# Kernel optimization log

Hardware: AMD Instinct MI355X
Metric: run time of the kernel (lower is better)

The kernel has to match this reference:

```python
import jax, jax.numpy as jnp
import numpy as np

NUM_HEADS = 8
LN_EPS = 1e-5


def setup_inputs() -> dict:
    key = jax.random.key(0)
    ks = jax.random.split(key, 5)
    B, C, H, W = 4, 256, 48, 48
    scale = 1.0 / np.sqrt(C)
    return {
        "x": jax.random.normal(ks[0], (B, C, H, W), dtype=jnp.float32),
        "Wq": jax.random.normal(ks[1], (C, C), dtype=jnp.float32) * scale,
        "Wk": jax.random.normal(ks[2], (C, C), dtype=jnp.float32) * scale,
        "Wv": jax.random.normal(ks[3], (C, C), dtype=jnp.float32) * scale,
        "Wo": jax.random.normal(ks[4], (C, C), dtype=jnp.float32) * scale,
        "gamma": jnp.ones((C,), dtype=jnp.float32),
        "beta": jnp.zeros((C,), dtype=jnp.float32),
    }


def reference(x, Wq, Wk, Wv, Wo, gamma, beta):
    B, C, H, W = x.shape
    hd = C // NUM_HEADS
    N = H * W
    xf = x.reshape(B, C, N)  # [B, C, N]
    # 1x1 conv (no bias) == channel matmul, then split heads: [B, h, d, N]
    def proj(Wm):
        return jnp.einsum('oc,bcn->bon', Wm, xf).reshape(B, NUM_HEADS, hd, N)
    q = proj(Wq)
    k = proj(Wk)
    v = proj(Wv)
    # scores[b,h,i,j] = sum_d q[b,h,d,i] k[b,h,d,j] / sqrt(hd)
    scores = jnp.einsum('bhdi,bhdj->bhij', q, k) / jnp.sqrt(jnp.float32(hd))
    attn = jax.nn.softmax(scores, axis=-1)  # [B, h, N, N]
    # attended[b,h,d,i] = sum_j v[b,h,d,j] attn[b,h,i,j]
    attended = jnp.einsum('bhdj,bhij->bhdi', v, attn).reshape(B, C, H, W)
    out = jnp.einsum('oc,bchw->bohw', Wo, attended) + x
    # LayerNorm over channels (applied in NHWC layout in original)
    mu = out.mean(axis=1, keepdims=True)
    var = out.var(axis=1, keepdims=True)
    out = (out - mu) * jax.lax.rsqrt(var + LN_EPS)
    out = out * gamma[None, :, None, None] + beta[None, :, None, None]
    return out
```

## Files before the change

### kernel.cpp

```cpp
#include <hip/hip_runtime.h>

#define DEVI __device__ __forceinline__

typedef __bf16 bf16x8 __attribute__((ext_vector_type(8)));
typedef float f32x4 __attribute__((ext_vector_type(4)));

#define QSCALE 0.25503488f

#if __has_builtin(__builtin_amdgcn_exp2f)
#define EXP2(x) __builtin_amdgcn_exp2f(x)
#else
#define EXP2(x) __expf(0.69314718055994531f * (x))
#endif

DEVI unsigned short bfbits(float f) {
  union { __bf16 h; unsigned short u; } x;
  x.h = (__bf16)f;
  return x.u;
}
DEVI unsigned packbf2(float a, float b) {
  return (unsigned)bfbits(a) | ((unsigned)bfbits(b) << 16);
}
DEVI float bflo(unsigned u) { return __uint_as_float(u << 16); }
DEVI float bfhi(unsigned u) { return __uint_as_float(u & 0xffff0000u); }

DEVI void gload16(const unsigned short* g, void* l) {
  __builtin_amdgcn_global_load_lds((__attribute__((address_space(1))) const unsigned*)g,
                                   (__attribute__((address_space(3))) unsigned*)l, 16, 0, 0);
}

__global__ __launch_bounds__(256) void k_prep_x(const float* __restrict__ x,
                                                unsigned short* __restrict__ xT) {
  __shared__ float tile[64][65];
  const int b = blockIdx.x, n0 = blockIdx.y * 64, c0 = blockIdx.z * 64;
  const int t = threadIdx.x, tn = t & 63, tg = t >> 6;
  const float* xp = x + ((size_t)b * 256 + c0) * 2304 + n0;
#pragma unroll
  for (int i = 0; i < 16; ++i) {
    const int c = tg * 16 + i;
    tile[c][tn] = xp[(size_t)c * 2304 + tn];
  }
  __syncthreads();
  unsigned short* op = xT + ((size_t)b * 2304 + n0) * 256 + c0;
#pragma unroll
  for (int i = 0; i < 16; ++i) {
    const int n = tg * 16 + i;
    op[(size_t)n * 256 + tn] = bfbits(tile[tn][n]);
  }
}

__global__ __launch_bounds__(256) void k_prep_w(const float* __restrict__ Wq,
                                                const float* __restrict__ Wk,
                                                const float* __restrict__ Wv,
                                                const float* __restrict__ Wo,
                                                unsigned short* __restrict__ dst) {
  const float* src = blockIdx.y == 0 ? Wq : blockIdx.y == 1 ? Wk : blockIdx.y == 2 ? Wv : Wo;
  unsigned short* d = dst + (size_t)blockIdx.y * 65536;
  const int i = (blockIdx.x * 256 + threadIdx.x) * 4;
  const float4 v = *(const float4*)(src + i);
  uint2 u;
  u.x = packbf2(v.x, v.y);
  u.y = packbf2(v.z, v.w);
  *(uint2*)(d + i) = u;
}

__global__ __launch_bounds__(256) void k_proj_qk(const unsigned short* __restrict__ xT,
                                                 const unsigned short* __restrict__ Wb,
                                                 unsigned short* __restrict__ qT,
                                                 unsigned short* __restrict__ kT) {
  __shared__ __align__(16) unsigned char wlds[16384];
  const unsigned short* W = Wb + (blockIdx.z ? 65536 : 0);
  unsigned short* outp = blockIdx.z ? kT : qT;
  const float scale = blockIdx.z ? 1.0f : QSCALE;
  const int l = threadIdx.x & 63, w = threadIdx.x >> 6;
  const int lr = l & 15, lg = l >> 4;
  const int row0 = blockIdx.x * 128 + w * 32;
  const int col0 = blockIdx.y * 32;
  {
    const int t = threadIdx.x;
    const int row = t >> 3;
    const int cj0 = (t & 7) * 4;
#pragma unroll
    for (int i = 0; i < 4; ++i) {
      const int cj = cj0 + i;
      const uint4 v = *(const uint4*)(W + (size_t)(col0 + row) * 256 + cj * 8);
      *(uint4*)(wlds + row * 512 + ((cj * 16) ^ ((row & 7) << 4))) = v;
    }
  }
  __syncthreads();

  f32x4 acc[2][2];
#pragma unroll
  for (int i = 0; i < 2; ++i)
#pragma unroll
    for (int j = 0; j < 2; ++j) acc[i][j] = (f32x4){0.f, 0.f, 0.f, 0.f};
  for (int ks = 0; ks < 8; ++ks) {
    const int c = ks * 32 + lg * 8;
    bf16x8 a[2], bfr[2];
#pragma unroll
    for (int nt = 0; nt < 2; ++nt)
      a[nt] = *(const bf16x8*)(xT + (size_t)(row0 + nt * 16 + lr) * 256 + c);
#pragma unroll
    for (int ot = 0; ot < 2; ++ot) {
      const int brow = ot * 16 + lr;
      bfr[ot] = *(const bf16x8*)(wlds + brow * 512 + (((ks * 4 + lg) * 16) ^ ((brow & 7) << 4)));
    }
#pragma unroll
    for (int nt = 0; nt < 2; ++nt)
#pragma unroll
      for (int ot = 0; ot < 2; ++ot)
        acc[nt][ot] = __builtin_amdgcn_mfma_f32_16x16x32_bf16(a[nt], bfr[ot], acc[nt][ot], 0, 0, 0);
  }
#pragma unroll
  for (int nt = 0; nt < 2; ++nt)
#pragma unroll
    for (int ot = 0; ot < 2; ++ot)
#pragma unroll
      for (int r = 0; r < 4; ++r) {
        const int n = row0 + nt * 16 + lg * 4 + r;
        const int o = col0 + ot * 16 + lr;
        outp[(size_t)n * 256 + o] = bfbits(acc[nt][ot][r] * scale);
      }
}

__global__ __launch_bounds__(256) void k_proj_v(const unsigned short* __restrict__ xT,
                                                const unsigned short* __restrict__ Wv,
                                                unsigned short* __restrict__ vN) {
  __shared__ __align__(16) unsigned char wlds[32768];
  const int l = threadIdx.x & 63, w = threadIdx.x >> 6;
  const int lr = l & 15, lg = l >> 4;
  const int rowbase = blockIdx.x * 64;
  const int col0 = blockIdx.y * 32;
  {
    const int t = threadIdx.x;
    const int row = t >> 2;
    const int cj0 = (t & 3) * 8;
#pragma unroll
    for (int i = 0; i < 8; ++i) {
      const int cj = cj0 + i;
      const uint4 v = *(const uint4*)(Wv + (size_t)(rowbase + row) * 256 + cj * 8);
      *(uint4*)(wlds + row * 512 + ((cj * 16) ^ ((row & 7) << 4))) = v;
    }
  }
  __syncthreads();

  f32x4 acc[2];
  acc[0] = (f32x4){0.f, 0.f, 0.f, 0.f};
  acc[1] = (f32x4){0.f, 0.f, 0.f, 0.f};
  for (int ks = 0; ks < 8; ++ks) {
    const int c = ks * 32 + lg * 8;
    bf16x8 a, bfr[2];
    const int arow = w * 16 + lr;
    a = *(const bf16x8*)(wlds + arow * 512 + (((ks * 4 + lg) * 16) ^ ((arow & 7) << 4)));
#pragma unroll
    for (int nt = 0; nt < 2; ++nt)
      bfr[nt] = *(const bf16x8*)(xT + (size_t)(col0 + nt * 16 + lr) * 256 + c);
#pragma unroll
    for (int nt = 0; nt < 2; ++nt)
      acc[nt] = __builtin_amdgcn_mfma_f32_16x16x32_bf16(a, bfr[nt], acc[nt], 0, 0, 0);
  }
  const int b = blockIdx.y / 72, nb = (blockIdx.y % 72) * 32;
#pragma unroll
  for (int nt = 0; nt < 2; ++nt)
#pragma unroll
    for (int r = 0; r < 4; ++r) {
      const int o = rowbase + w * 16 + lg * 4 + r;
      const int n = nb + nt * 16 + lr;
      vN[(size_t)b * 589824 + (size_t)o * 2304 + n] = bfbits(acc[nt][r]);
    }
}

template <bool DIRECT>
__global__ __launch_bounds__(256) void k_attn(const unsigned short* __restrict__ qT,
                                              const unsigned short* __restrict__ kT,
                                              const unsigned short* __restrict__ vN,
                                              unsigned short* __restrict__ partO,
                                              float* __restrict__ partS,
                                              unsigned short* __restrict__ attT,
                                              int tpc) {
  __shared__ __align__(16) unsigned char sm[32768];
  const int l = threadIdx.x & 63, w = threadIdx.x >> 6;
  const int lr = l & 15, lg = l >> 4;
  const int bh = blockIdx.y, b = bh >> 3, h = bh & 7;
  const int i0 = blockIdx.x * 128 + w * 32;
  const int c = blockIdx.z, t0 = c * tpc;
  unsigned char* smw = sm + w * 4096;

  bf16x8 qf[2];
#pragma unroll
  for (int it = 0; it < 2; ++it)
    qf[it] = *(const bf16x8*)(qT + (size_t)(b * 2304 + i0 + it * 16 + lr) * 256 + h * 32 + lg * 8);

  bf16x8 ones;
#pragma unroll
  for (int e = 0; e < 8; ++e) ones[e] = (__bf16)1.0f;

  f32x4 oacc[2][2];
#pragma unroll
  for (int i = 0; i < 2; ++i)
#pragma unroll
    for (int j = 0; j < 2; ++j) oacc[i][j] = (f32x4){0.f, 0.f, 0.f, 0.f};
  f32x4 psum[2];
  psum[0] = (f32x4){0.f, 0.f, 0.f, 0.f};
  psum[1] = (f32x4){0.f, 0.f, 0.f, 0.f};

  const unsigned short* ksrc = kT + (size_t)(b * 2304 + l) * 256 + h * 32 + w * 8;
  const int vks = w >> 1;
  const int vlg = (w * 2 + (l >> 5)) & 3;
  const unsigned short* vsrc = vN + (size_t)(b * 256 + h * 32 + (l & 31)) * 2304 + vks * 32 + vlg * 8;
  const int kdst = 16384 + w * 1024;
  const int vdst = 24576 + w * 1024;

  gload16(ksrc + (size_t)t0 * 16384, sm + kdst);
  gload16(vsrc + t0 * 64, sm + vdst);
  __syncthreads();

  for (int tt = 0; tt < tpc; ++tt) {
    const int buf = tt & 1;
    if (tt < tpc - 1) {
      const int nbuf = (tt + 1) & 1;
      gload16(ksrc + (size_t)(t0 + tt + 1) * 16384, sm + kdst + nbuf * 4096);
      gload16(vsrc + (t0 + tt + 1) * 64, sm + vdst + nbuf * 4096);
    }

    const unsigned char* kb = sm + 16384 + buf * 4096;
    const unsigned char* vb = sm + 24576 + buf * 4096;

    bf16x8 kf[4];
#pragma unroll
    for (int jt = 0; jt < 4; ++jt)
      kf[jt] = *(const bf16x8*)(kb + lg * 1024 + (jt * 16 + lr) * 16);

    f32x4 s[4][2];
    const f32x4 zf = (f32x4){0.f, 0.f, 0.f, 0.f};
#pragma unroll
    for (int jt = 0; jt < 4; ++jt)
#pragma unroll
      for (int it = 0; it < 2; ++it)
        s[jt][it] = __builtin_amdgcn_mfma_f32_16x16x32_bf16(kf[jt], qf[it], zf, 0, 0, 0);

#pragma unroll
    for (int it = 0; it < 2; ++it) {
      const int iloc = it * 16 + lr;
      const unsigned swz = (unsigned)((iloc & 7) << 4);
      unsigned char* prow = smw + iloc * 128;
#pragma unroll
      for (int jt = 0; jt < 4; ++jt) {
        const float p0 = EXP2(s[jt][it][0]);
        const float p1 = EXP2(s[jt][it][1]);
        const float p2 = EXP2(s[jt][it][2]);
        const float p3 = EXP2(s[jt][it][3]);
        const unsigned jb = (unsigned)(jt * 32 + lg * 8);
        uint2 u;
        u.x = packbf2(p0, p1);
        u.y = packbf2(p2, p3);
        *(uint2*)(prow + (jb ^ swz)) = u;
      }
    }

    bf16x8 vf[2][2], pf[2][2];
#pragma unroll
    for (int dt = 0; dt < 2; ++dt)
#pragma unroll
      for (int ks = 0; ks < 2; ++ks)
        vf[dt][ks] = *(const bf16x8*)(vb + ks * 2048 + lg * 512 + (dt * 16 + lr) * 16);
#pragma unroll
    for (int it = 0; it < 2; ++it) {
      const int iloc = it * 16 + lr;
      const unsigned swz = (unsigned)((iloc & 7) << 4);
#pragma unroll
      for (int ks = 0; ks < 2; ++ks)
        pf[it][ks] = *(const bf16x8*)(smw + iloc * 128 + ((unsigned)(ks * 64 + lg * 16) ^ swz));
    }
#pragma unroll
    for (int dt = 0; dt < 2; ++dt)
#pragma unroll
      for (int it = 0; it < 2; ++it) {
        oacc[dt][it] = __builtin_amdgcn_mfma_f32_16x16x32_bf16(vf[dt][0], pf[it][0], oacc[dt][it], 0, 0, 0);
        oacc[dt][it] = __builtin_amdgcn_mfma_f32_16x16x32_bf16(vf[dt][1], pf[it][1], oacc[dt][it], 0, 0, 0);
      }
#pragma unroll
    for (int it = 0; it < 2; ++it) {
      psum[it] = __builtin_amdgcn_mfma_f32_16x16x32_bf16(ones, pf[it][0], psum[it], 0, 0, 0);
      psum[it] = __builtin_amdgcn_mfma_f32_16x16x32_bf16(ones, pf[it][1], psum[it], 0, 0, 0);
    }
    __syncthreads();
  }

  if (DIRECT) {
#pragma unroll
    for (int it = 0; it < 2; ++it) {
      const float inv = 1.0f / psum[it][0];
      const int iloc = it * 16 + lr;
      unsigned char* orow = smw + iloc * 68;
#pragma unroll
      for (int dt = 0; dt < 2; ++dt) {
        const int d = dt * 16 + lg * 4;
        *(unsigned*)(orow + d * 2) = packbf2(oacc[dt][it][0] * inv, oacc[dt][it][1] * inv);
        *(unsigned*)(orow + d * 2 + 4) = packbf2(oacc[dt][it][2] * inv, oacc[dt][it][3] * inv);
      }
    }
    __syncthreads();
    unsigned* attu = (unsigned*)attT;
#pragma unroll
    for (int it2 = 0; it2 < 8; ++it2) {
      const int lin = it2 * 64 + l;
      const int row = lin >> 4, k = lin & 15;
      const unsigned u = *(const unsigned*)(smw + row * 68 + k * 4);
      attu[(size_t)(b * 2304 + i0 + row) * 128 + h * 16 + k] = u;
    }
  } else {
    const size_t pbase = ((size_t)(c * 32 + bh) * 2304 + i0) * 32;
#pragma unroll
    for (int it = 0; it < 2; ++it)
#pragma unroll
      for (int dt = 0; dt < 2; ++dt) {
        const size_t addr = pbase + (size_t)(it * 16 + lr) * 32 + dt * 16 + lg * 4;
        uint2 u;
        u.x = packbf2(oacc[dt][it][0], oacc[dt][it][1]);
        u.y = packbf2(oacc[dt][it][2], oacc[dt][it][3]);
        *(uint2*)(partO + addr) = u;
      }
    if (lg == 0) {
      const size_t sbase = (size_t)(c * 32 + bh) * 2304 + i0;
      partS[sbase + lr] = psum[0][0];
      partS[sbase + 16 + lr] = psum[1][0];
    }
  }
}

__global__ __launch_bounds__(256) void k_combine(const unsigned short* __restrict__ partO,
                                                 const float* __restrict__ partS,
                                                 unsigned short* __restrict__ attT,
                                                 int nc) {
  const int bid = blockIdx.x;
  const int bh = bid / 36, i0 = (bid % 36) * 64;
  const int b = bh >> 3, h = bh & 7;
  const int tid = threadIdx.x;
  const int dq = tid & 3, di = tid >> 2;
  const int i = i0 + di;

  float ssum = 0.f;
  for (int c = 0; c < nc; ++c) ssum += partS[(size_t)(c * 32 + bh) * 2304 + i];
  const float inv = 1.0f / ssum;

  float acc[8];
#pragma unroll
  for (int e = 0; e < 8; ++e) acc[e] = 0.f;
  for (int c = 0; c < nc; ++c) {
    const uint4 v = *(const uint4*)(partO + (((size_t)(c * 32 + bh) * 2304 + i) * 32 + dq * 8));
    acc[0] += bflo(v.x); acc[1] += bfhi(v.x);
    acc[2] += bflo(v.y); acc[3] += bfhi(v.y);
    acc[4] += bflo(v.z); acc[5] += bfhi(v.z);
    acc[6] += bflo(v.w); acc[7] += bfhi(v.w);
  }
  uint4 o;
  o.x = packbf2(acc[0] * inv, acc[1] * inv);
  o.y = packbf2(acc[2] * inv, acc[3] * inv);
  o.z = packbf2(acc[4] * inv, acc[5] * inv);
  o.w = packbf2(acc[6] * inv, acc[7] * inv);
  unsigned* attu = (unsigned*)attT;
  *(uint4*)(attu + (size_t)(b * 2304 + i) * 128 + h * 16 + dq * 4) = o;
}

__global__ __launch_bounds__(256) void k_out_ln(const unsigned short* __restrict__ Wo,
                                                const unsigned short* __restrict__ attT,
                                                const float* __restrict__ x,
                                                const float* __restrict__ gamma,
                                                const float* __restrict__ beta,
                                                float* __restrict__ out) {
  __shared__ __align__(16) unsigned char alds[8192];
  __shared__ float wsum[4][16], wsq[4][16], smean[16], srstd[16];
  const int l = threadIdx.x & 63, w = threadIdx.x >> 6;
  const int lr = l & 15, lg = l >> 4;
  const int b = blockIdx.x / 144;
  const int n0 = (blockIdx.x % 144) * 16;
  const int row0 = w * 64;
  const size_t bn0 = (size_t)b * 2304 + n0;
  {
    const int t = threadIdx.x;
    const int row = t >> 4;
    const int cj0 = (t & 15) * 2;
#pragma unroll
    for (int i = 0; i < 2; ++i) {
      const int cj = cj0 + i;
      const uint4 v = *(const uint4*)(attT + (bn0 + row) * 256 + cj * 8);
      *(uint4*)(alds + row * 512 + ((cj * 16) ^ ((row & 7) << 4))) = v;
    }
  }
  __syncthreads();

  f32x4 acc[4];
#pragma unroll
  for (int i = 0; i < 4; ++i) acc[i] = (f32x4){0.f, 0.f, 0.f, 0.f};
  for (int ks = 0; ks < 8; ++ks) {
    const int c = ks * 32 + lg * 8;
    bf16x8 a[4], bb;
#pragma unroll
    for (int rt = 0; rt < 4; ++rt)
      a[rt] = *(const bf16x8*)(Wo + (size_t)(row0 + rt * 16 + lr) * 256 + c);
    bb = *(const bf16x8*)(alds + lr * 512 + (((ks * 4 + lg) * 16) ^ ((lr & 7) << 4)));
#pragma unroll
    for (int rt = 0; rt < 4; ++rt)
      acc[rt] = __builtin_amdgcn_mfma_f32_16x16x32_bf16(a[rt], bb, acc[rt], 0, 0, 0);
  }
  const float* xb = x + (size_t)b * 589824;
  float vals[4][4];
  float s0 = 0.f, q0 = 0.f;
#pragma unroll
  for (int rt = 0; rt < 4; ++rt)
#pragma unroll
    for (int r = 0; r < 4; ++r) {
      const int o = row0 + rt * 16 + lg * 4 + r;
      const int n = n0 + lr;
      const float vv = acc[rt][r] + xb[(size_t)o * 2304 + n];
      vals[rt][r] = vv;
      s0 += vv;
      q0 += vv * vv;
    }
  s0 += __shfl_xor(s0, 16); s0 += __shfl_xor(s0, 32);
  q0 += __shfl_xor(q0, 16); q0 += __shfl_xor(q0, 32);
  if (l < 16) {
    wsum[w][l] = s0;
    wsq[w][l] = q0;
  }
  __syncthreads();
  if (threadIdx.x < 16) {
    const int c16 = threadIdx.x;
    const float S = wsum[0][c16] + wsum[1][c16] + wsum[2][c16] + wsum[3][c16];
    const float Q = wsq[0][c16] + wsq[1][c16] + wsq[2][c16] + wsq[3][c16];
    const float mean = S * (1.0f / 256.0f);
    const float var = Q * (1.0f / 256.0f) - mean * mean;
    smean[c16] = mean;
    srstd[c16] = rsqrtf(var + 1e-5f);
  }
  __syncthreads();
  {
    const float mean = smean[lr];
    const float rstd = srstd[lr];
    const int n = n0 + lr;
#pragma unroll
    for (int rt = 0; rt < 4; ++rt)
#pragma unroll
      for (int r = 0; r < 4; ++r) {
        const int o = row0 + rt * 16 + lg * 4 + r;
        out[(size_t)b * 589824 + (size_t)o * 2304 + n] =
            (vals[rt][r] - mean) * rstd * gamma[o] + beta[o];
      }
  }
}

extern "C" void kernel_launch(void* const* d_in, const int* in_sizes, int n_in,
                              void* d_out, int out_size, void* d_ws, size_t ws_size,
                              hipStream_t stream) {
  (void)in_sizes; (void)n_in; (void)out_size;
  const float* x = (const float*)d_in[0];
  const float* Wq = (const float*)d_in[1];
  const float* Wk = (const float*)d_in[2];
  const float* Wv = (const float*)d_in[3];
  const float* Wo = (const float*)d_in[4];
  const float* gamma = (const float*)d_in[5];
  const float* beta = (const float*)d_in[6];
  float* out = (float*)d_out;
  char* ws = (char*)d_ws;
  unsigned short* attT = (unsigned short*)(ws);
  unsigned short* Wb = (unsigned short*)(ws + 4718592);
  unsigned short* qT = (unsigned short*)(ws + 5242880);
  unsigned short* kT = (unsigned short*)(ws + 9961472);
  unsigned short* vN = (unsigned short*)(ws + 14680064);
  unsigned short* xT = (unsigned short*)(ws + 19398656);

  const size_t base = 19398656;
  const size_t need4 = base + 4ull * (4718592 + 294912);
  const size_t need2 = base + 2ull * (4718592 + 294912);
  const int nc = (ws_size >= need4) ? 4 : (ws_size >= need2) ? 2 : 1;
  unsigned short* partO = (unsigned short*)(ws + base);
  float* partS = (float*)(ws + base + (size_t)nc * 4718592);

  k_prep_x<<<dim3(4, 36, 4), 256, 0, stream>>>(x, xT);
  k_prep_w<<<dim3(64, 4), 256, 0, stream>>>(Wq, Wk, Wv, Wo, Wb);
  k_proj_qk<<<dim3(72, 8, 2), 256, 0, stream>>>(xT, Wb, qT, kT);
  k_proj_v<<<dim3(4, 288), 256, 0, stream>>>(xT, Wb + 2 * 65536, vN);
  if (nc > 1) {
    k_attn<false><<<dim3(18, 32, nc), 256, 0, stream>>>(qT, kT, vN, partO, partS, attT, 36 / nc);
    k_combine<<<dim3(1152), 256, 0, stream>>>(partO, partS, attT, nc);
  } else {
    k_attn<true><<<dim3(18, 32, 1), 256, 0, stream>>>(qT, kT, vN, attT, (float*)attT, attT, 36);
  }
  k_out_ln<<<dim3(576), 256, 0, stream>>>(Wb + 3 * 65536, attT, x, gamma, beta, out);
}
```

Measured before the change: 168.4 us.

## Fuse weight conversion into projections, head-major Q/K, fold combine into output LN

Drops the separate weight-prep kernel: Q/K/V projections now read fp32 weights and convert them to bf16 while staging into LDS. Q and K are written head-major ([b,h,n,32]) so attention loads contiguous K tiles, with an XOR swizzle on the LDS reads. The split-K combine kernel is folded into the output-projection/LayerNorm kernel, which reduces the partial outputs and sums directly into its LDS tile. This cuts two launches and the intermediate attT round trip. The cost is redundant weight conversion across blocks, redundant combine reads, and a small Wo conversion kernel reusing the q buffer after attention.

```diff
diff --git a/kernel.cpp b/kernel.cpp
--- a/kernel.cpp
+++ b/kernel.cpp
@@ -49,42 +49,45 @@
   }
 }
 
-__global__ __launch_bounds__(256) void k_prep_w(const float* __restrict__ Wq,
-                                                const float* __restrict__ Wk,
-                                                const float* __restrict__ Wv,
-                                                const float* __restrict__ Wo,
-                                                unsigned short* __restrict__ dst) {
-  const float* src = blockIdx.y == 0 ? Wq : blockIdx.y == 1 ? Wk : blockIdx.y == 2 ? Wv : Wo;
-  unsigned short* d = dst + (size_t)blockIdx.y * 65536;
+__global__ __launch_bounds__(256) void k_prep_wo(const float* __restrict__ Wo,
+                                                 unsigned short* __restrict__ WoB) {
   const int i = (blockIdx.x * 256 + threadIdx.x) * 4;
-  const float4 v = *(const float4*)(src + i);
+  const float4 v = *(const float4*)(Wo + i);
   uint2 u;
   u.x = packbf2(v.x, v.y);
   u.y = packbf2(v.z, v.w);
-  *(uint2*)(d + i) = u;
+  *(uint2*)(WoB + i) = u;
 }
 
 __global__ __launch_bounds__(256) void k_proj_qk(const unsigned short* __restrict__ xT,
-                                                 const unsigned short* __restrict__ Wb,
-                                                 unsigned short* __restrict__ qT,
-                                                 unsigned short* __restrict__ kT) {
-  __shared__ __align__(16) unsigned char wlds[16384];
-  const unsigned short* W = Wb + (blockIdx.z ? 65536 : 0);
-  unsigned short* outp = blockIdx.z ? kT : qT;
-  const float scale = blockIdx.z ? 1.0f : QSCALE;
+                                                 const float* __restrict__ Wq,
+                                                 const float* __restrict__ Wk,
+                                                 unsigned short* __restrict__ qhm,
+                                                 unsigned short* __restrict__ khm) {
+  __shared__ __align__(16) unsigned char wlds[32768];
   const int l = threadIdx.x & 63, w = threadIdx.x >> 6;
   const int lr = l & 15, lg = l >> 4;
-  const int row0 = blockIdx.x * 128 + w * 32;
-  const int col0 = blockIdx.y * 32;
+  const int row0 = blockIdx.x * 64 + w * 16;
+  const int h = blockIdx.y;
   {
     const int t = threadIdx.x;
-    const int row = t >> 3;
-    const int cj0 = (t & 7) * 4;
-#pragma unroll
-    for (int i = 0; i < 4; ++i) {
+    const int mat = t >> 7;
+    const int t2 = t & 127;
+    const int row = t2 >> 2;
+    const int cj0 = (t2 & 3) * 8;
+    const float* wp = (mat ? Wk : Wq) + (size_t)(h * 32 + row) * 256;
+    unsigned char* ldst = wlds + mat * 16384 + row * 512;
+#pragma unroll
+    for (int i = 0; i < 8; ++i) {
       const int cj = cj0 + i;
-      const uint4 v = *(const uint4*)(W + (size_t)(col0 + row) * 256 + cj * 8);
-      *(uint4*)(wlds + row * 512 + ((cj * 16) ^ ((row & 7) << 4))) = v;
+      const float4 v0 = *(const float4*)(wp + cj * 8);
+      const float4 v1 = *(const float4*)(wp + cj * 8 + 4);
+      uint4 u;
+      u.x = packbf2(v0.x, v0.y);
+      u.y = packbf2(v0.z, v0.w);
+      u.z = packbf2(v1.x, v1.y);
+      u.w = packbf2(v1.z, v1.w);
+      *(uint4*)(ldst + ((cj * 16) ^ ((row & 7) << 4))) = u;
     }
   }
   __syncthreads();
@@ -96,35 +99,41 @@
     for (int j = 0; j < 2; ++j) acc[i][j] = (f32x4){0.f, 0.f, 0.f, 0.f};
   for (int ks = 0; ks < 8; ++ks) {
     const int c = ks * 32 + lg * 8;
-    bf16x8 a[2], bfr[2];
-#pragma unroll
-    for (int nt = 0; nt < 2; ++nt)
-      a[nt] = *(const bf16x8*)(xT + (size_t)(row0 + nt * 16 + lr) * 256 + c);
+    const bf16x8 a = *(const bf16x8*)(xT + (size_t)(row0 + lr) * 256 + c);
+    bf16x8 bfr[2][2];
 #pragma unroll
     for (int ot = 0; ot < 2; ++ot) {
       const int brow = ot * 16 + lr;
-      bfr[ot] = *(const bf16x8*)(wlds + brow * 512 + (((ks * 4 + lg) * 16) ^ ((brow & 7) << 4)));
-    }
-#pragma unroll
-    for (int nt = 0; nt < 2; ++nt)
+      const unsigned off = (unsigned)(brow * 512) + (((unsigned)((ks * 4 + lg) * 16)) ^ ((brow & 7) << 4));
+      bfr[0][ot] = *(const bf16x8*)(wlds + off);
+      bfr[1][ot] = *(const bf16x8*)(wlds + 16384 + off);
+    }
+#pragma unroll
+    for (int m = 0; m < 2; ++m)
 #pragma unroll
       for (int ot = 0; ot < 2; ++ot)
-        acc[nt][ot] = __builtin_amdgcn_mfma_f32_16x16x32_bf16(a[nt], bfr[ot], acc[nt][ot], 0, 0, 0);
-  }
-#pragma unroll
-  for (int nt = 0; nt < 2; ++nt)
+        acc[m][ot] = __builtin_amdgcn_mfma_f32_16x16x32_bf16(a, bfr[m][ot], acc[m][ot], 0, 0, 0);
+  }
+  const int b = row0 / 2304;
+  const int nloc = row0 - b * 2304;
+  const size_t slab = (size_t)(b * 8 + h) * 2304;
+#pragma unroll
+  for (int m = 0; m < 2; ++m) {
+    unsigned short* outp = m ? khm : qhm;
+    const float scale = m ? 1.0f : QSCALE;
 #pragma unroll
     for (int ot = 0; ot < 2; ++ot)
 #pragma unroll
       for (int r = 0; r < 4; ++r) {
-        const int n = row0 + nt * 16 + lg * 4 + r;
-        const int o = col0 + ot * 16 + lr;
-        outp[(size_t)n * 256 + o] = bfbits(acc[nt][ot][r] * scale);
-      }
+        const int n = nloc + lg * 4 + r;
+        const int d = ot * 16 + lr;
+        outp[(slab + n) * 32 + d] = bfbits(acc[m][ot][r] * scale);
+      }
+  }
 }
 
 __global__ __launch_bounds__(256) void k_proj_v(const unsigned short* __restrict__ xT,
-                                                const unsigned short* __restrict__ Wv,
+                                                const float* __restrict__ Wv,
                                                 unsigned short* __restrict__ vN) {
   __shared__ __align__(16) unsigned char wlds[32768];
   const int l = threadIdx.x & 63, w = threadIdx.x >> 6;
@@ -135,11 +144,19 @@
     const int t = threadIdx.x;
     const int row = t >> 2;
     const int cj0 = (t & 3) * 8;
+    const float* wp = Wv + (size_t)(rowbase + row) * 256;
+    unsigned char* ldst = wlds + row * 512;
 #pragma unroll
     for (int i = 0; i < 8; ++i) {
       const int cj = cj0 + i;
-      const uint4 v = *(const uint4*)(Wv + (size_t)(rowbase + row) * 256 + cj * 8);
-      *(uint4*)(wlds + row * 512 + ((cj * 16) ^ ((row & 7) << 4))) = v;
+      const float4 v0 = *(const float4*)(wp + cj * 8);
+      const float4 v1 = *(const float4*)(wp + cj * 8 + 4);
+      uint4 u;
+      u.x = packbf2(v0.x, v0.y);
+      u.y = packbf2(v0.z, v0.w);
+      u.z = packbf2(v1.x, v1.y);
+      u.w = packbf2(v1.z, v1.w);
+      *(uint4*)(ldst + ((cj * 16) ^ ((row & 7) << 4))) = u;
     }
   }
   __syncthreads();
@@ -151,7 +168,7 @@
     const int c = ks * 32 + lg * 8;
     bf16x8 a, bfr[2];
     const int arow = w * 16 + lr;
-    a = *(const bf16x8*)(wlds + arow * 512 + (((ks * 4 + lg) * 16) ^ ((arow & 7) << 4)));
+    a = *(const bf16x8*)(wlds + arow * 512 + (((unsigned)((ks * 4 + lg) * 16)) ^ ((arow & 7) << 4)));
 #pragma unroll
     for (int nt = 0; nt < 2; ++nt)
       bfr[nt] = *(const bf16x8*)(xT + (size_t)(col0 + nt * 16 + lr) * 256 + c);
@@ -171,8 +188,8 @@
 }
 
 template <bool DIRECT>
-__global__ __launch_bounds__(256) void k_attn(const unsigned short* __restrict__ qT,
-                                              const unsigned short* __restrict__ kT,
+__global__ __launch_bounds__(256) void k_attn(const unsigned short* __restrict__ qhm,
+                                              const unsigned short* __restrict__ khm,
                                               const unsigned short* __restrict__ vN,
                                               unsigned short* __restrict__ partO,
                                               float* __restrict__ partS,
@@ -185,11 +202,15 @@
   const int i0 = blockIdx.x * 128 + w * 32;
   const int c = blockIdx.z, t0 = c * tpc;
   unsigned char* smw = sm + w * 4096;
+  const size_t slab = (size_t)bh * 2304;
 
   bf16x8 qf[2];
-#pragma unroll
-  for (int it = 0; it < 2; ++it)
-    qf[it] = *(const bf16x8*)(qT + (size_t)(b * 2304 + i0 + it * 16 + lr) * 256 + h * 32 + lg * 8);
+  {
+    const unsigned short* qbase = qhm + (slab + i0) * 32;
+#pragma unroll
+    for (int it = 0; it < 2; ++it)
+      qf[it] = *(const bf16x8*)(qbase + (it * 16 + lr) * 32 + lg * 8);
+  }
 
   bf16x8 ones;
 #pragma unroll
@@ -204,14 +225,15 @@
   psum[0] = (f32x4){0.f, 0.f, 0.f, 0.f};
   psum[1] = (f32x4){0.f, 0.f, 0.f, 0.f};
 
-  const unsigned short* ksrc = kT + (size_t)(b * 2304 + l) * 256 + h * 32 + w * 8;
+  const unsigned short* kbase = khm + slab * 32 + (size_t)(64 * w + (l ^ ((l >> 2) & 3))) * 8;
   const int vks = w >> 1;
   const int vlg = (w * 2 + (l >> 5)) & 3;
   const unsigned short* vsrc = vN + (size_t)(b * 256 + h * 32 + (l & 31)) * 2304 + vks * 32 + vlg * 8;
   const int kdst = 16384 + w * 1024;
   const int vdst = 24576 + w * 1024;
-
-  gload16(ksrc + (size_t)t0 * 16384, sm + kdst);
+  const int kxor = ((lg ^ (lr & 3)) << 4);
+
+  gload16(kbase + (size_t)t0 * 2048, sm + kdst);
   gload16(vsrc + t0 * 64, sm + vdst);
   __syncthreads();
 
@@ -219,7 +241,7 @@
     const int buf = tt & 1;
     if (tt < tpc - 1) {
       const int nbuf = (tt + 1) & 1;
-      gload16(ksrc + (size_t)(t0 + tt + 1) * 16384, sm + kdst + nbuf * 4096);
+      gload16(kbase + (size_t)(t0 + tt + 1) * 2048, sm + kdst + nbuf * 4096);
       gload16(vsrc + (t0 + tt + 1) * 64, sm + vdst + nbuf * 4096);
     }
 
@@ -227,9 +249,12 @@
     const unsigned char* vb = sm + 24576 + buf * 4096;
 
     bf16x8 kf[4];
-#pragma unroll
-    for (int jt = 0; jt < 4; ++jt)
-      kf[jt] = *(const bf16x8*)(kb + lg * 1024 + (jt * 16 + lr) * 16);
+    {
+      const unsigned char* kread = kb + lr * 64 + kxor;
+#pragma unroll
+      for (int jt = 0; jt < 4; ++jt)
+        kf[jt] = *(const bf16x8*)(kread + jt * 1024);
+    }
 
     f32x4 s[4][2];
     const f32x4 zf = (f32x4){0.f, 0.f, 0.f, 0.f};
@@ -329,42 +354,12 @@
   }
 }
 
-__global__ __launch_bounds__(256) void k_combine(const unsigned short* __restrict__ partO,
-                                                 const float* __restrict__ partS,
-                                                 unsigned short* __restrict__ attT,
-                                                 int nc) {
-  const int bid = blockIdx.x;
-  const int bh = bid / 36, i0 = (bid % 36) * 64;
-  const int b = bh >> 3, h = bh & 7;
-  const int tid = threadIdx.x;
-  const int dq = tid & 3, di = tid >> 2;
-  const int i = i0 + di;
-
-  float ssum = 0.f;
-  for (int c = 0; c < nc; ++c) ssum += partS[(size_t)(c * 32 + bh) * 2304 + i];
-  const float inv = 1.0f / ssum;
-
-  float acc[8];
-#pragma unroll
-  for (int e = 0; e < 8; ++e) acc[e] = 0.f;
-  for (int c = 0; c < nc; ++c) {
-    const uint4 v = *(const uint4*)(partO + (((size_t)(c * 32 + bh) * 2304 + i) * 32 + dq * 8));
-    acc[0] += bflo(v.x); acc[1] += bfhi(v.x);
-    acc[2] += bflo(v.y); acc[3] += bfhi(v.y);
-    acc[4] += bflo(v.z); acc[5] += bfhi(v.z);
-    acc[6] += bflo(v.w); acc[7] += bfhi(v.w);
-  }
-  uint4 o;
-  o.x = packbf2(acc[0] * inv, acc[1] * inv);
-  o.y = packbf2(acc[2] * inv, acc[3] * inv);
-  o.z = packbf2(acc[4] * inv, acc[5] * inv);
-  o.w = packbf2(acc[6] * inv, acc[7] * inv);
-  unsigned* attu = (unsigned*)attT;
-  *(uint4*)(attu + (size_t)(b * 2304 + i) * 128 + h * 16 + dq * 4) = o;
-}
-
+template <bool COMBINE>
 __global__ __launch_bounds__(256) void k_out_ln(const unsigned short* __restrict__ Wo,
                                                 const unsigned short* __restrict__ attT,
+                                                const unsigned short* __restrict__ partO,
+                                                const float* __restrict__ partS,
+                                                int nc,
                                                 const float* __restrict__ x,
                                                 const float* __restrict__ gamma,
                                                 const float* __restrict__ beta,
@@ -377,13 +372,44 @@
   const int n0 = (blockIdx.x % 144) * 16;
   const int row0 = w * 64;
   const size_t bn0 = (size_t)b * 2304 + n0;
-  {
+
+  if (COMBINE) {
+    const int t = threadIdx.x;
+    const int row = t >> 4;
+    const int i = n0 + row;
+    const int cj0 = (t & 15) * 2;
+#pragma unroll
+    for (int ii = 0; ii < 2; ++ii) {
+      const int cj = cj0 + ii;
+      const int h = cj >> 2;
+      const int d0 = (cj & 3) * 8;
+      const int bh8 = b * 8 + h;
+      float ssum = 0.f;
+      float a0 = 0.f, a1 = 0.f, a2 = 0.f, a3 = 0.f, a4 = 0.f, a5 = 0.f, a6 = 0.f, a7 = 0.f;
+      for (int cz = 0; cz < nc; ++cz) {
+        const size_t rbase = (size_t)(cz * 32 + bh8) * 2304 + i;
+        ssum += partS[rbase];
+        const uint4 v = *(const uint4*)(partO + rbase * 32 + d0);
+        a0 += bflo(v.x); a1 += bfhi(v.x);
+        a2 += bflo(v.y); a3 += bfhi(v.y);
+        a4 += bflo(v.z); a5 += bfhi(v.z);
+        a6 += bflo(v.w); a7 += bfhi(v.w);
+      }
+      const float inv = 1.0f / ssum;
+      uint4 u;
+      u.x = packbf2(a0 * inv, a1 * inv);
+      u.y = packbf2(a2 * inv, a3 * inv);
+      u.z = packbf2(a4 * inv, a5 * inv);
+      u.w = packbf2(a6 * inv, a7 * inv);
+      *(uint4*)(alds + row * 512 + ((cj * 16) ^ ((row & 7) << 4))) = u;
+    }
+  } else {
     const int t = threadIdx.x;
     const int row = t >> 4;
     const int cj0 = (t & 15) * 2;
 #pragma unroll
-    for (int i = 0; i < 2; ++i) {
-      const int cj = cj0 + i;
+    for (int ii = 0; ii < 2; ++ii) {
+      const int cj = cj0 + ii;
       const uint4 v = *(const uint4*)(attT + (bn0 + row) * 256 + cj * 8);
       *(uint4*)(alds + row * 512 + ((cj * 16) ^ ((row & 7) << 4))) = v;
     }
@@ -399,7 +425,7 @@
 #pragma unroll
     for (int rt = 0; rt < 4; ++rt)
       a[rt] = *(const bf16x8*)(Wo + (size_t)(row0 + rt * 16 + lr) * 256 + c);
-    bb = *(const bf16x8*)(alds + lr * 512 + (((ks * 4 + lg) * 16) ^ ((lr & 7) << 4)));
+    bb = *(const bf16x8*)(alds + lr * 512 + (((unsigned)((ks * 4 + lg) * 16)) ^ ((lr & 7) << 4)));
 #pragma unroll
     for (int rt = 0; rt < 4; ++rt)
       acc[rt] = __builtin_amdgcn_mfma_f32_16x16x32_bf16(a[rt], bb, acc[rt], 0, 0, 0);
@@ -464,28 +490,30 @@
   float* out = (float*)d_out;
   char* ws = (char*)d_ws;
   unsigned short* attT = (unsigned short*)(ws);
-  unsigned short* Wb = (unsigned short*)(ws + 4718592);
-  unsigned short* qT = (unsigned short*)(ws + 5242880);
-  unsigned short* kT = (unsigned short*)(ws + 9961472);
-  unsigned short* vN = (unsigned short*)(ws + 14680064);
-  unsigned short* xT = (unsigned short*)(ws + 19398656);
-
-  const size_t base = 19398656;
-  const size_t need4 = base + 4ull * (4718592 + 294912);
-  const size_t need2 = base + 2ull * (4718592 + 294912);
+  unsigned short* qhm = (unsigned short*)(ws + 4718592);
+  unsigned short* khm = (unsigned short*)(ws + 9437184);
+  unsigned short* vN = (unsigned short*)(ws + 14155776);
+  unsigned short* xT = (unsigned short*)(ws + 18874368);
+  unsigned short* WoB = qhm;
+
+  const size_t base = 18874368;
+  const size_t chunk = 4718592 + 294912;
+  const size_t need4 = base + 4 * chunk;
+  const size_t need2 = base + 2 * chunk;
   const int nc = (ws_size >= need4) ? 4 : (ws_size >= need2) ? 2 : 1;
   unsigned short* partO = (unsigned short*)(ws + base);
   float* partS = (float*)(ws + base + (size_t)nc * 4718592);
 
   k_prep_x<<<dim3(4, 36, 4), 256, 0, stream>>>(x, xT);
-  k_prep_w<<<dim3(64, 4), 256, 0, stream>>>(Wq, Wk, Wv, Wo, Wb);
-  k_proj_qk<<<dim3(72, 8, 2), 256, 0, stream>>>(xT, Wb, qT, kT);
-  k_proj_v<<<dim3(4, 288), 256, 0, stream>>>(xT, Wb + 2 * 65536, vN);
+  k_proj_qk<<<dim3(144, 8), 256, 0, stream>>>(xT, Wq, Wk, qhm, khm);
+  k_proj_v<<<dim3(4, 288), 256, 0, stream>>>(xT, Wv, vN);
   if (nc > 1) {
-    k_attn<false><<<dim3(18, 32, nc), 256, 0, stream>>>(qT, kT, vN, partO, partS, attT, 36 / nc);
-    k_combine<<<dim3(1152), 256, 0, stream>>>(partO, partS, attT, nc);
+    k_attn<false><<<dim3(18, 32, nc), 256, 0, stream>>>(qhm, khm, vN, partO, partS, attT, 36 / nc);
+    k_prep_wo<<<dim3(64), 256, 0, stream>>>(Wo, WoB);
+    k_out_ln<true><<<dim3(576), 256, 0, stream>>>(WoB, attT, partO, partS, nc, x, gamma, beta, out);
   } else {
-    k_attn<true><<<dim3(18, 32, 1), 256, 0, stream>>>(qT, kT, vN, attT, (float*)attT, attT, 36);
-  }
-  k_out_ln<<<dim3(576), 256, 0, stream>>>(Wb + 3 * 65536, attT, x, gamma, beta, out);
-}
+    k_attn<true><<<dim3(18, 32, 1), 256, 0, stream>>>(qhm, khm, vN, attT, (float*)attT, attT, 36);
+    k_prep_wo<<<dim3(64), 256, 0, stream>>>(Wo, WoB);
+    k_out_ln<false><<<dim3(576), 256, 0, stream>>>(WoB, attT, partO, partS, 1, x, gamma, beta, out);
+  }
+}
```

Result: no change. 171.3 us (+1.7%).
